# Kernel tuning notes

Measured on AMD Instinct MI355X. Metric: run time of the kernel, lower is better.

## Reference

```python
import jax, jax.numpy as jnp
import numpy as np

B, N, C = 4, 4096, 1024
NUM_HEADS = 16
HEAD_DIM = C // NUM_HEADS


def setup_inputs() -> dict:
    key = jax.random.key(0)
    k1, k2, k3, k4 = jax.random.split(key, 4)
    s_in = 1.0 / np.sqrt(C)
    return {
        "x": jax.random.normal(k1, (B, N, C), dtype=jnp.float32),
        "H": 64,
        "W": 64,
        "Wqkv": jax.random.normal(k2, (3 * C, C), dtype=jnp.float32) * s_in,
        "Wproj": jax.random.normal(k3, (C, C), dtype=jnp.float32) * s_in,
        "bproj": jnp.zeros((C,), dtype=jnp.float32),
        "alpha": jnp.ones((NUM_HEADS,), dtype=jnp.float32),
    }


def reference(x, H, W, Wqkv, Wproj, bproj, alpha):
    Bb, Nn, Cc = x.shape
    h, d = NUM_HEADS, HEAD_DIM
    # qkv: [B, N, 3C] -> [3, B, h, N, d]
    qkv = jnp.einsum('bnc,oc->bno', x, Wqkv)
    qkv = qkv.reshape(Bb, Nn, 3, h, d).transpose(2, 0, 3, 1, 4)
    q, k, v = qkv[0], qkv[1], qkv[2]  # each [B, h, N, d]
    # channel attention: contract over tokens N -> [B, h, d, d]
    attn = jnp.einsum('bhnd,bhne->bhde', k, q) / alpha[None, :, None, None]
    attn = jax.nn.softmax(attn, axis=-1)
    # (dropout is identity in eval/reference mode)
    # head_out: [B, h, d, N] -> transpose -> [B, N, h, d] -> concat heads
    out = jnp.einsum('bhde,bhne->bhdn', attn, v)
    out = out.transpose(0, 3, 1, 2).reshape(Bb, Nn, Cc)
    return jnp.einsum('bnc,oc->bno', out, Wproj) + bproj
```

## Files before the change

### kernel.cpp

```cpp
#include <hip/hip_runtime.h>
#include <hip/hip_bf16.h>
#include <cstdint>
#include <cstddef>

typedef unsigned short u16;
typedef __bf16 bf16x8 __attribute__((ext_vector_type(8)));
typedef float f32x4 __attribute__((ext_vector_type(4)));
typedef unsigned short u16x4 __attribute__((ext_vector_type(4)));
typedef unsigned short u16x8 __attribute__((ext_vector_type(8)));

#define AS1(p) ((__attribute__((address_space(1))) void*)(p))
#define AS3(p) ((__attribute__((address_space(3))) void*)(p))

__device__ __forceinline__ float bf2f(u16 u) {
  unsigned v = ((unsigned)u) << 16; float f; __builtin_memcpy(&f, &v, 4); return f;
}
__device__ __forceinline__ u16 f2bf(float f) {
  unsigned u; __builtin_memcpy(&u, &f, 4);
  u += 0x7FFFu + ((u >> 16) & 1u);
  return (u16)(u >> 16);
}

__global__ __launch_bounds__(256) void convert_kernel(const float* __restrict__ src,
                                                      u16* __restrict__ dst, int n4) {
  int i = blockIdx.x * blockDim.x + threadIdx.x;
  int stride = gridDim.x * blockDim.x;
  for (; i < n4; i += stride) {
    float4 v = ((const float4*)src)[i];
    u16x4 o;
    o.x = f2bf(v.x); o.y = f2bf(v.y); o.z = f2bf(v.z); o.w = f2bf(v.w);
    ((u16x4*)dst)[i] = o;
  }
}

__global__ __launch_bounds__(256) void convert_split_kernel(const float* __restrict__ src,
                                                            u16* __restrict__ hi,
                                                            u16* __restrict__ lo, int n4) {
  int i = blockIdx.x * blockDim.x + threadIdx.x;
  int stride = gridDim.x * blockDim.x;
  for (; i < n4; i += stride) {
    float4 v = ((const float4*)src)[i];
    u16x4 oh, ol;
    oh.x = f2bf(v.x); ol.x = f2bf(v.x - bf2f(oh.x));
    oh.y = f2bf(v.y); ol.y = f2bf(v.y - bf2f(oh.y));
    oh.z = f2bf(v.z); ol.z = f2bf(v.z - bf2f(oh.z));
    oh.w = f2bf(v.w); ol.w = f2bf(v.w - bf2f(oh.w));
    ((u16x4*)hi)[i] = oh;
    ((u16x4*)lo)[i] = ol;
  }
}

__global__ __launch_bounds__(256) void transpose_split_kernel(const float* __restrict__ x,
                                                              u16* __restrict__ Xb,
                                                              u16* __restrict__ XThi,
                                                              u16* __restrict__ XTlo) {
  __shared__ u16 lhi[64 * 72];
  __shared__ u16 llo[64 * 72];
  const int t  = threadIdx.x;
  const int nT = blockIdx.x, cT = blockIdx.y, b = blockIdx.z;
  const size_t xbase = ((size_t)b * 4096 + nT * 64) * 1024 + cT * 64;
  const int c4 = (t & 15) * 4;
  const int r0 = t >> 4;
  const int rot_w = (t & 3) << 4;
#pragma unroll
  for (int j = 0; j < 4; ++j) {
    int r = r0 + j * 16;
    float4 v = *(const float4*)(x + xbase + (size_t)r * 1024 + c4);
    u16x4 hi;
    hi.x = f2bf(v.x); hi.y = f2bf(v.y); hi.z = f2bf(v.z); hi.w = f2bf(v.w);
    *(u16x4*)(Xb + xbase + (size_t)r * 1024 + c4) = hi;
    u16 lo[4];
    lo[0] = f2bf(v.x - bf2f(hi.x)); lo[1] = f2bf(v.y - bf2f(hi.y));
    lo[2] = f2bf(v.z - bf2f(hi.z)); lo[3] = f2bf(v.w - bf2f(hi.w));
    u16 hia[4] = { hi.x, hi.y, hi.z, hi.w };
    const int rs = r ^ rot_w;
#pragma unroll
    for (int i = 0; i < 4; ++i) {
      lhi[(c4 + i) * 72 + rs] = hia[i];
      llo[(c4 + i) * 72 + rs] = lo[i];
    }
  }
  __syncthreads();
  const int c  = t >> 2;
  const int n0 = (t & 3) * 16;
  const int rot_r = ((t >> 4) & 3) << 4;
  const int nA = n0 ^ rot_r;
  const size_t tbase = ((size_t)b * 1024 + cT * 64 + c) * 4096 + nT * 64 + n0;
  *(u16x8*)(XThi + tbase)     = *(const u16x8*)(lhi + c * 72 + nA);
  *(u16x8*)(XThi + tbase + 8) = *(const u16x8*)(lhi + c * 72 + nA + 8);
  *(u16x8*)(XTlo + tbase)     = *(const u16x8*)(llo + c * 72 + nA);
  *(u16x8*)(XTlo + tbase + 8) = *(const u16x8*)(llo + c * 72 + nA + 8);
}

template<bool OUT_BF16, bool HAS_BIAS>
__global__ __launch_bounds__(512, 2) void gemm_pipe(const u16* __restrict__ A,
                                                    const u16* __restrict__ B,
                                                    void* __restrict__ Cv,
                                                    const float* __restrict__ bias,
                                                    int M, int N, int K,
                                                    size_t sA, size_t sB, size_t sC) {
  __shared__ __align__(16) u16 lds[4][2][8192];
  const int tid  = threadIdx.x;
  const int lane = tid & 63;
  const int wave = tid >> 6;
  const int wm = wave >> 2, wn = wave & 3;
  const int rowTile = blockIdx.x * 256;
  const int colTile = blockIdx.y * 256;
  A += (size_t)blockIdx.z * sA;
  B += (size_t)blockIdx.z * sB;

  size_t srcA[2], srcB[2];
  int ldsOff[2];
#pragma unroll
  for (int j = 0; j < 2; ++j) {
    const int L = j * 512 + tid;
    const int sr = L >> 3;
    const int slot = (L & 7) ^ (sr & 7);
    const int r  = (sr << 1) | (slot >> 2);
    const int kq = slot & 3;
    srcA[j] = (size_t)(rowTile + r) * K + kq * 8;
    srcB[j] = (size_t)(colTile + r) * K + kq * 8;
    ldsOff[j] = (j * 512 + (tid & 448)) * 16;
  }

  const int m15 = lane & 15, kq4 = lane >> 4;
  const int r0a = wm * 128 + m15, sa0 = r0a >> 1;
  const int idxA0 = sa0 * 64 + (((((r0a & 1) << 2) | kq4)) ^ (sa0 & 7)) * 8;
  const int r0b = wn * 64 + m15, sb0 = r0b >> 1;
  const int idxB0 = sb0 * 64 + (((((r0b & 1) << 2) | kq4)) ^ (sb0 & 7)) * 8;

  const int NT = K >> 5;

  auto stageA = [&](int tt) {
    char* d = (char*)&lds[tt & 3][0][0];
    const int kt = tt << 5;
#pragma unroll
    for (int j = 0; j < 2; ++j)
      __builtin_amdgcn_global_load_lds(AS1(A + srcA[j] + kt), AS3(d + ldsOff[j]), 16, 0, 0);
  };
  auto stageB = [&](int tt) {
    char* d = (char*)&lds[tt & 3][1][0];
    const int kt = tt << 5;
#pragma unroll
    for (int j = 0; j < 2; ++j)
      __builtin_amdgcn_global_load_lds(AS1(B + srcB[j] + kt), AS3(d + ldsOff[j]), 16, 0, 0);
  };

  stageA(0); stageB(0);
  if (NT > 1) { stageA(1); stageB(1); }
  if (NT > 2) { stageA(2); stageB(2); }
  if (NT > 2) asm volatile("s_waitcnt vmcnt(8)" ::: "memory");
  else        asm volatile("s_waitcnt vmcnt(0)" ::: "memory");
  __builtin_amdgcn_sched_barrier(0);
  __builtin_amdgcn_s_barrier();
  __builtin_amdgcn_sched_barrier(0);

  f32x4 acc[8][4] = {};
  for (int t = 0; t < NT; ++t) {
    const u16* bufA = &lds[t & 3][0][0];
    const u16* bufB = &lds[t & 3][1][0];
    bf16x8 a[8], bfr[4];
#pragma unroll
    for (int ni = 0; ni < 4; ++ni) bfr[ni] = *(const bf16x8*)(bufB + idxB0 + ni * 512);
#pragma unroll
    for (int mi = 0; mi < 4; ++mi) a[mi] = *(const bf16x8*)(bufA + idxA0 + mi * 512);
    if (t + 3 < NT) stageA(t + 3);
    __builtin_amdgcn_sched_barrier(0);
    __builtin_amdgcn_s_barrier();
    __builtin_amdgcn_sched_barrier(0);
    __builtin_amdgcn_s_setprio(1);
#pragma unroll
    for (int mi = 0; mi < 4; ++mi)
#pragma unroll
      for (int ni = 0; ni < 4; ++ni)
        acc[mi][ni] = __builtin_amdgcn_mfma_f32_16x16x32_bf16(a[mi], bfr[ni], acc[mi][ni], 0, 0, 0);
    __builtin_amdgcn_s_setprio(0);
    __builtin_amdgcn_sched_barrier(0);
    __builtin_amdgcn_s_barrier();
    __builtin_amdgcn_sched_barrier(0);
#pragma unroll
    for (int mi = 4; mi < 8; ++mi) a[mi] = *(const bf16x8*)(bufA + idxA0 + mi * 512);
    if (t + 3 < NT) stageB(t + 3);
    __builtin_amdgcn_sched_barrier(0);
    __builtin_amdgcn_s_barrier();
    __builtin_amdgcn_sched_barrier(0);
    __builtin_amdgcn_s_setprio(1);
#pragma unroll
    for (int mi = 4; mi < 8; ++mi)
#pragma unroll
      for (int ni = 0; ni < 4; ++ni)
        acc[mi][ni] = __builtin_amdgcn_mfma_f32_16x16x32_bf16(a[mi], bfr[ni], acc[mi][ni], 0, 0, 0);
    __builtin_amdgcn_s_setprio(0);
    if (t < NT - 1) {
      if (t + 3 < NT)      asm volatile("s_waitcnt vmcnt(8)" ::: "memory");
      else if (t + 2 < NT) asm volatile("s_waitcnt vmcnt(4)" ::: "memory");
      else                 asm volatile("s_waitcnt vmcnt(0)" ::: "memory");
    }
    __builtin_amdgcn_sched_barrier(0);
    __builtin_amdgcn_s_barrier();
    __builtin_amdgcn_sched_barrier(0);
  }

  const int crow0 = rowTile + wm * 128 + (lane >> 4) * 4;
  const int ccol0 = colTile + wn * 64 + m15;
  if constexpr (OUT_BF16) {
    u16* C = (u16*)Cv + (size_t)blockIdx.z * sC;
#pragma unroll
    for (int mi = 0; mi < 8; ++mi)
#pragma unroll
      for (int ni = 0; ni < 4; ++ni) {
        const int col = ccol0 + ni * 16;
        const float bv = HAS_BIAS ? bias[col] : 0.f;
#pragma unroll
        for (int r = 0; r < 4; ++r)
          C[(size_t)(crow0 + mi * 16 + r) * N + col] = f2bf(acc[mi][ni][r] + bv);
      }
  } else {
    float* C = (float*)Cv + (size_t)blockIdx.z * sC;
#pragma unroll
    for (int mi = 0; mi < 8; ++mi)
#pragma unroll
      for (int ni = 0; ni < 4; ++ni) {
        const int col = ccol0 + ni * 16;
        const float bv = HAS_BIAS ? bias[col] : 0.f;
#pragma unroll
        for (int r = 0; r < 4; ++r)
          C[(size_t)(crow0 + mi * 16 + r) * N + col] = acc[mi][ni][r] + bv;
      }
  }
}

template<int L>
__device__ __forceinline__ void pipe4k_core(const u16* __restrict__ pAh,
                                            const u16* __restrict__ pAl,
                                            const u16* __restrict__ pBh,
                                            const u16* __restrict__ pBl,
                                            u16* lds, int ldsByteOff,
                                            int idxA0, int idxB0, int bOff,
                                            int NT, int half,
                                            f32x4 acc[4][4]) {
  auto stage = [&](int tt) {
    u16* d = lds + (tt & 3) * 16384;
    const int kt = tt << 5;
    __builtin_amdgcn_global_load_lds(AS1(pAh + kt), AS3((char*)d + ldsByteOff), 16, 0, 0);
    __builtin_amdgcn_global_load_lds(AS1(pAl + kt), AS3((char*)(d + 4096) + ldsByteOff), 16, 0, 0);
    if constexpr (L == 4) {
      __builtin_amdgcn_global_load_lds(AS1(pBh + kt), AS3((char*)(d + 8192) + ldsByteOff), 16, 0, 0);
      __builtin_amdgcn_global_load_lds(AS1(pBl + kt), AS3((char*)(d + 12288) + ldsByteOff), 16, 0, 0);
    }
  };

  stage(0); stage(1); stage(2); stage(3);
  if constexpr (L == 4) asm volatile("s_waitcnt vmcnt(8)" ::: "memory");
  else                  asm volatile("s_waitcnt vmcnt(4)" ::: "memory");
  __builtin_amdgcn_sched_barrier(0);
  __builtin_amdgcn_s_barrier();
  __builtin_amdgcn_sched_barrier(0);

  const int npairs = NT >> 1;
  for (int i = 0; i < npairs; ++i) {
    const u16* base = lds + ((2 * i + half) & 3) * 16384;
    bf16x8 ah[4], al[4], bh[4], bl[4];
#pragma unroll
    for (int ni = 0; ni < 4; ++ni) {
      bh[ni] = *(const bf16x8*)(base + bOff + idxB0 + ni * 512);
      bl[ni] = *(const bf16x8*)(base + bOff + 4096 + idxB0 + ni * 512);
    }
    ah[0] = *(const bf16x8*)(base + idxA0);
    ah[1] = *(const bf16x8*)(base + idxA0 + 512);
    al[0] = *(const bf16x8*)(base + 4096 + idxA0);
    al[1] = *(const bf16x8*)(base + 4096 + idxA0 + 512);
    __builtin_amdgcn_sched_barrier(0);
    __builtin_amdgcn_s_barrier();
    __builtin_amdgcn_sched_barrier(0);
    __builtin_amdgcn_s_setprio(1);
#pragma unroll
    for (int mi = 0; mi < 2; ++mi)
#pragma unroll
      for (int ni = 0; ni < 4; ++ni) {
        acc[mi][ni] = __builtin_amdgcn_mfma_f32_16x16x32_bf16(ah[mi], bh[ni], acc[mi][ni], 0, 0, 0);
        acc[mi][ni] = __builtin_amdgcn_mfma_f32_16x16x32_bf16(ah[mi], bl[ni], acc[mi][ni], 0, 0, 0);
        acc[mi][ni] = __builtin_amdgcn_mfma_f32_16x16x32_bf16(al[mi], bh[ni], acc[mi][ni], 0, 0, 0);
      }
    __builtin_amdgcn_s_setprio(0);
    __builtin_amdgcn_sched_barrier(0);
    __builtin_amdgcn_s_barrier();
    __builtin_amdgcn_sched_barrier(0);
    ah[2] = *(const bf16x8*)(base + idxA0 + 1024);
    ah[3] = *(const bf16x8*)(base + idxA0 + 1536);
    al[2] = *(const bf16x8*)(base + 4096 + idxA0 + 1024);
    al[3] = *(const bf16x8*)(base + 4096 + idxA0 + 1536);
    __builtin_amdgcn_sched_barrier(0);
    __builtin_amdgcn_s_barrier();
    __builtin_amdgcn_sched_barrier(0);
    if (i + 2 < npairs) { stage(2 * i + 4); stage(2 * i + 5); }
    __builtin_amdgcn_sched_barrier(0);
    __builtin_amdgcn_s_setprio(1);
#pragma unroll
    for (int mi = 2; mi < 4; ++mi)
#pragma unroll
      for (int ni = 0; ni < 4; ++ni) {
        acc[mi][ni] = __builtin_amdgcn_mfma_f32_16x16x32_bf16(ah[mi], bh[ni], acc[mi][ni], 0, 0, 0);
        acc[mi][ni] = __builtin_amdgcn_mfma_f32_16x16x32_bf16(ah[mi], bl[ni], acc[mi][ni], 0, 0, 0);
        acc[mi][ni] = __builtin_amdgcn_mfma_f32_16x16x32_bf16(al[mi], bh[ni], acc[mi][ni], 0, 0, 0);
      }
    __builtin_amdgcn_s_setprio(0);
    if (i < npairs - 1) {
      if (i + 2 < npairs) {
        if constexpr (L == 4) asm volatile("s_waitcnt vmcnt(8)" ::: "memory");
        else                  asm volatile("s_waitcnt vmcnt(4)" ::: "memory");
      } else {
        asm volatile("s_waitcnt vmcnt(0)" ::: "memory");
      }
    }
    __builtin_amdgcn_sched_barrier(0);
    __builtin_amdgcn_s_barrier();
    __builtin_amdgcn_sched_barrier(0);
  }
}

__global__ __launch_bounds__(512, 2) void gram_pipe(const u16* __restrict__ XThi,
                                                    const u16* __restrict__ XTlo,
                                                    float* __restrict__ Gpart) {
  __shared__ __align__(16) u16 ldsmem[4 * 4 * 4096];
  const int tid = threadIdx.x, lane = tid & 63, wave = tid >> 6;
  const int q = wave & 3, half = wave >> 2;
  const int qm = q >> 1, qn = q & 1;
  const int bid = blockIdx.x;
  int b, rT, cT, slice, k0, NT; bool same = false;
  if (bid < 64) {
    b = bid & 3; const int j2 = bid >> 2;
    rT = cT = j2 >> 1; slice = j2 & 1; k0 = slice * 2048; NT = 64; same = true;
  } else {
    const int e = bid - 64; b = e & 3;
    const int idx = e >> 2; const int tile = idx >> 2, kq = idx & 3;
    int t = tile, rt = 0;
    while (t >= 7 - rt) { t -= 7 - rt; ++rt; }
    const int ct = rt + 1 + t;
    rT = rt; cT = ct;
    if (kq >= 2) { rT = ct; cT = rt; }
    slice = kq & 1; k0 = kq * 1024; NT = 32;
  }
  const int rowTile = rT * 128, colTile = cT * 128;
  const u16* Ah = XThi + ((size_t)b << 22);
  const u16* Al = XTlo + ((size_t)b << 22);

  const int sr = tid >> 3;
  const int slot = (tid & 7) ^ (sr & 7);
  const int r = (sr << 1) | (slot >> 2);
  const int kq8 = (slot & 3) * 8;
  const u16* pAh = Ah + (size_t)(rowTile + r) * 4096 + k0 + kq8;
  const u16* pAl = Al + (size_t)(rowTile + r) * 4096 + k0 + kq8;
  const u16* pBh = Ah + (size_t)(colTile + r) * 4096 + k0 + kq8;
  const u16* pBl = Al + (size_t)(colTile + r) * 4096 + k0 + kq8;
  const int ldsByteOff = (tid & 448) * 16;

  const int m15 = lane & 15, kq4 = lane >> 4;
  const int r0a = qm * 64 + m15, sa0 = r0a >> 1;
  const int idxA0 = sa0 * 64 + (((((r0a & 1) << 2) | kq4)) ^ (sa0 & 7)) * 8;
  const int r0b = qn * 64 + m15, sb0 = r0b >> 1;
  const int idxB0 = sb0 * 64 + (((((r0b & 1) << 2) | kq4)) ^ (sb0 & 7)) * 8;

  f32x4 acc[4][4] = {};
  if (same) pipe4k_core<2>(pAh, pAl, pAh, pAl, ldsmem, ldsByteOff, idxA0, idxB0, 0, NT, half, acc);
  else      pipe4k_core<4>(pAh, pAl, pBh, pBl, ldsmem, ldsByteOff, idxA0, idxB0, 8192, NT, half, acc);

  float* red = (float*)ldsmem;
  const int rr = (lane >> 4) * 4;
  if (half) {
#pragma unroll
    for (int mi = 0; mi < 4; ++mi)
#pragma unroll
      for (int ni = 0; ni < 4; ++ni)
        *(f32x4*)(red + q * 4352 + (ni * 16 + m15) * 68 + mi * 16 + rr) = acc[mi][ni];
  }
  __syncthreads();
  if (!half) {
    float* out = Gpart + ((size_t)(slice * 4 + b) << 20);
    const int crow0 = rowTile + qm * 64 + rr;
    const int ccol0 = colTile + qn * 64 + m15;
#pragma unroll
    for (int mi = 0; mi < 4; ++mi)
#pragma unroll
      for (int ni = 0; ni < 4; ++ni) {
        f32x4 v = *(const f32x4*)(red + q * 4352 + (ni * 16 + m15) * 68 + mi * 16 + rr);
        v += acc[mi][ni];
#pragma unroll
        for (int r4 = 0; r4 < 4; ++r4)
          out[(size_t)(crow0 + mi * 16 + r4) * 1024 + ccol0 + ni * 16] = v[r4];
      }
  }
}

__global__ __launch_bounds__(256) void gram_reduce_split(const float* __restrict__ Gp,
                                                         u16* __restrict__ Ghi,
                                                         u16* __restrict__ Glo) {
  const int rt = blockIdx.x, ct = blockIdx.y, b = blockIdx.z;
  const bool diag128 = (rt >> 1) == (ct >> 1);
  const float* s0 = Gp + ((size_t)b << 20);
  const float* s1 = Gp + ((size_t)(4 + b) << 20);
  __shared__ float lT[64 * 68];
  const int t = threadIdx.x;
  const int r = t >> 2;
  const int c16 = (t & 3) * 16;

  if (!diag128) {
    const size_t bb = (size_t)(ct * 64 + r) * 1024 + rt * 64 + c16;
#pragma unroll
    for (int q = 0; q < 4; ++q) {
      float4 v0 = *(const float4*)(s0 + bb + q * 4);
      float4 v1 = *(const float4*)(s1 + bb + q * 4);
      float4 s = { v0.x + v1.x, v0.y + v1.y, v0.z + v1.z, v0.w + v1.w };
      *(float4*)(lT + r * 68 + c16 + q * 4) = s;
    }
    __syncthreads();
  }

  const size_t ab = (size_t)(rt * 64 + r) * 1024 + ct * 64 + c16;
  const size_t ob = ((size_t)b << 20) + ab;
#pragma unroll
  for (int q = 0; q < 4; ++q) {
    float4 v0 = *(const float4*)(s0 + ab + q * 4);
    float4 v1 = *(const float4*)(s1 + ab + q * 4);
    float g[4] = { v0.x + v1.x, v0.y + v1.y, v0.z + v1.z, v0.w + v1.w };
    if (!diag128) {
#pragma unroll
      for (int i = 0; i < 4; ++i) g[i] += lT[(c16 + q * 4 + i) * 68 + r];
    }
    u16x4 oh, ol;
    oh.x = f2bf(g[0]); ol.x = f2bf(g[0] - bf2f(oh.x));
    oh.y = f2bf(g[1]); ol.y = f2bf(g[1] - bf2f(oh.y));
    oh.z = f2bf(g[2]); ol.z = f2bf(g[2] - bf2f(oh.z));
    oh.w = f2bf(g[3]); ol.w = f2bf(g[3] - bf2f(oh.w));
    *(u16x4*)(Ghi + ob + q * 4) = oh;
    *(u16x4*)(Glo + ob + q * 4) = ol;
  }
}

__global__ __launch_bounds__(512, 2) void tprime_pipe(const u16* __restrict__ Wqh,
                                                      const u16* __restrict__ Wql,
                                                      const u16* __restrict__ Ghi,
                                                      const u16* __restrict__ Glo,
                                                      u16* __restrict__ Tph,
                                                      u16* __restrict__ Tpl) {
  __shared__ __align__(16) u16 ldsmem[4 * 4 * 4096];
  const int tid = threadIdx.x, lane = tid & 63, wave = tid >> 6;
  const int q = wave & 3, half = wave >> 2;
  const int qm = q >> 1, qn = q & 1;
  const int bid = blockIdx.x;
  const int b = bid & 3, tile = bid >> 2;
  const int rowTile = (tile >> 3) * 128, colTile = (tile & 7) * 128;
  const size_t zoff = (size_t)b << 20;

  const int sr = tid >> 3;
  const int slot = (tid & 7) ^ (sr & 7);
  const int r = (sr << 1) | (slot >> 2);
  const int kq8 = (slot & 3) * 8;
  const u16* pAh = Wqh + (size_t)(rowTile + r) * 1024 + kq8;
  const u16* pAl = Wql + (size_t)(rowTile + r) * 1024 + kq8;
  const u16* pBh = Ghi + zoff + (size_t)(colTile + r) * 1024 + kq8;
  const u16* pBl = Glo + zoff + (size_t)(colTile + r) * 1024 + kq8;
  const int ldsByteOff = (tid & 448) * 16;

  const int m15 = lane & 15, kq4 = lane >> 4;
  const int r0a = qm * 64 + m15, sa0 = r0a >> 1;
  const int idxA0 = sa0 * 64 + (((((r0a & 1) << 2) | kq4)) ^ (sa0 & 7)) * 8;
  const int r0b = qn * 64 + m15, sb0 = r0b >> 1;
  const int idxB0 = sb0 * 64 + (((((r0b & 1) << 2) | kq4)) ^ (sb0 & 7)) * 8;

  f32x4 acc[4][4] = {};
  pipe4k_core<4>(pAh, pAl, pBh, pBl, ldsmem, ldsByteOff, idxA0, idxB0, 8192, 32, half, acc);

  float* red = (float*)ldsmem;
  const int rr = (lane >> 4) * 4;
  if (half) {
#pragma unroll
    for (int mi = 0; mi < 4; ++mi)
#pragma unroll
      for (int ni = 0; ni < 4; ++ni)
        *(f32x4*)(red + q * 4352 + (ni * 16 + m15) * 68 + mi * 16 + rr) = acc[mi][ni];
  }
  __syncthreads();
  if (!half) {
    const int crow0 = rowTile + qm * 64 + rr;
    const int ccol0 = colTile + qn * 64 + m15;
#pragma unroll
    for (int mi = 0; mi < 4; ++mi)
#pragma unroll
      for (int ni = 0; ni < 4; ++ni) {
        f32x4 v = *(const f32x4*)(red + q * 4352 + (ni * 16 + m15) * 68 + mi * 16 + rr);
        v += acc[mi][ni];
#pragma unroll
        for (int r4 = 0; r4 < 4; ++r4) {
          float x = v[r4];
          u16 hi = f2bf(x);
          u16 lo = f2bf(x - bf2f(hi));
          size_t off = zoff + (size_t)(crow0 + mi * 16 + r4) * 1024 + ccol0 + ni * 16;
          Tph[off] = hi;
          Tpl[off] = lo;
        }
      }
  }
}

__global__ __launch_bounds__(256) void s_softmax_kernel(const u16* __restrict__ Wqh,
                                                        const u16* __restrict__ Wql,
                                                        const u16* __restrict__ Tph,
                                                        const u16* __restrict__ Tpl,
                                                        const float* __restrict__ alpha,
                                                        u16* __restrict__ attnT) {
  const int h = blockIdx.x, b = blockIdx.y;
  const int tid = threadIdx.x, lane = tid & 63, wave = tid >> 6;
  __shared__ __align__(16) u16 lAh[64 * 32];
  __shared__ __align__(16) u16 lAl[64 * 32];
  __shared__ __align__(16) u16 lBh[64 * 32];
  __shared__ __align__(16) u16 lBl[64 * 32];

  const size_t aBase = (size_t)(1024 + h * 64) * 1024;
  const size_t bBase = ((size_t)b << 20) + (size_t)(h * 64) * 1024;

  f32x4 acc[4] = {};
  const int m  = lane & 15;
  const int ko = (lane >> 4) * 8;
  const int srow = tid >> 2;
  const int skc  = (tid & 3) * 8;
  const int ldsOff = (tid & 192) * 16;

  for (int kt = 0; kt < 1024; kt += 32) {
    __builtin_amdgcn_global_load_lds(AS1(Wqh + aBase + (size_t)srow * 1024 + kt + skc),
                                     AS3((char*)lAh + ldsOff), 16, 0, 0);
    __builtin_amdgcn_global_load_lds(AS1(Wql + aBase + (size_t)srow * 1024 + kt + skc),
                                     AS3((char*)lAl + ldsOff), 16, 0, 0);
    __builtin_amdgcn_global_load_lds(AS1(Tph + bBase + (size_t)srow * 1024 + kt + skc),
                                     AS3((char*)lBh + ldsOff), 16, 0, 0);
    __builtin_amdgcn_global_load_lds(AS1(Tpl + bBase + (size_t)srow * 1024 + kt + skc),
                                     AS3((char*)lBl + ldsOff), 16, 0, 0);
    __syncthreads();
    bf16x8 ah = *(const bf16x8*)(lAh + (wave * 16 + m) * 32 + ko);
    bf16x8 al = *(const bf16x8*)(lAl + (wave * 16 + m) * 32 + ko);
#pragma unroll
    for (int cb = 0; cb < 4; ++cb) {
      bf16x8 bh = *(const bf16x8*)(lBh + (cb * 16 + m) * 32 + ko);
      bf16x8 bl = *(const bf16x8*)(lBl + (cb * 16 + m) * 32 + ko);
      acc[cb] = __builtin_amdgcn_mfma_f32_16x16x32_bf16(ah, bh, acc[cb], 0, 0, 0);
      acc[cb] = __builtin_amdgcn_mfma_f32_16x16x32_bf16(ah, bl, acc[cb], 0, 0, 0);
      acc[cb] = __builtin_amdgcn_mfma_f32_16x16x32_bf16(al, bh, acc[cb], 0, 0, 0);
    }
    __syncthreads();
  }

  const float invA = 1.f / alpha[h];
  const int g = lane >> 4;
  const size_t obase = (size_t)(b * 16 + h) * 4096;
#pragma unroll
  for (int r = 0; r < 4; ++r) {
    int d = wave * 16 + g * 4 + r;
    float s[4];
#pragma unroll
    for (int cb = 0; cb < 4; ++cb) s[cb] = acc[cb][r] * invA;
    float mx = fmaxf(fmaxf(s[0], s[1]), fmaxf(s[2], s[3]));
#pragma unroll
    for (int o = 1; o < 16; o <<= 1) mx = fmaxf(mx, __shfl_xor(mx, o, 64));
    float e[4]; float sum = 0.f;
#pragma unroll
    for (int cb = 0; cb < 4; ++cb) { e[cb] = __expf(s[cb] - mx); sum += e[cb]; }
#pragma unroll
    for (int o = 1; o < 16; o <<= 1) sum += __shfl_xor(sum, o, 64);
    float inv = 1.f / sum;
#pragma unroll
    for (int cb = 0; cb < 4; ++cb) {
      int e_idx = cb * 16 + (lane & 15);
      attnT[obase + (size_t)e_idx * 64 + d] = f2bf(e[cb] * inv);
    }
  }
}

__global__ __launch_bounds__(256) void m_build_kernel(const u16* __restrict__ Wpb,
                                                      const u16* __restrict__ attnT,
                                                      u16* __restrict__ Mb) {
  const int oT = blockIdx.x, h = blockIdx.y, b = blockIdx.z;
  const int tid = threadIdx.x, lane = tid & 63, wave = tid >> 6;
  __shared__ __align__(16) u16 lA[128 * 64];
  __shared__ __align__(16) u16 lB[64 * 64];
  const int bh = b * 16 + h;
#pragma unroll
  for (int i = 0; i < 4; ++i) {
    int idx = i * 256 + tid;
    int row = idx >> 3;
    int kc  = (idx & 7) * 8;
    int ldsOff = (i * 256 + (tid & 192)) * 16;
    __builtin_amdgcn_global_load_lds(AS1(Wpb + (size_t)(oT * 128 + row) * 1024 + h * 64 + kc),
                                     AS3((char*)lA + ldsOff), 16, 0, 0);
  }
#pragma unroll
  for (int i = 0; i < 2; ++i) {
    int idx = i * 256 + tid;
    int ldsOff = (i * 256 + (tid & 192)) * 16;
    __builtin_amdgcn_global_load_lds(AS1(attnT + (size_t)bh * 4096 + idx * 8),
                                     AS3((char*)lB + ldsOff), 16, 0, 0);
  }
  __syncthreads();
  const int m  = lane & 15;
  const int ko = (lane >> 4) * 8;
  const int wr = wave * 32;
  f32x4 acc[2][4] = {};
#pragma unroll
  for (int ks = 0; ks < 2; ++ks) {
#pragma unroll
    for (int rb = 0; rb < 2; ++rb) {
      bf16x8 a = *(const bf16x8*)(lA + (wr + rb * 16 + m) * 64 + ks * 32 + ko);
#pragma unroll
      for (int cb = 0; cb < 4; ++cb) {
        bf16x8 bb = *(const bf16x8*)(lB + (cb * 16 + m) * 64 + ks * 32 + ko);
        acc[rb][cb] = __builtin_amdgcn_mfma_f32_16x16x32_bf16(a, bb, acc[rb][cb], 0, 0, 0);
      }
    }
  }
  u16* out = Mb + ((size_t)b << 20);
#pragma unroll
  for (int rb = 0; rb < 2; ++rb)
#pragma unroll
    for (int cb = 0; cb < 4; ++cb) {
      int col = h * 64 + cb * 16 + (lane & 15);
#pragma unroll
      for (int r = 0; r < 4; ++r) {
        int row = oT * 128 + wr + rb * 16 + (lane >> 4) * 4 + r;
        out[(size_t)row * 1024 + col] = f2bf(acc[rb][cb][r]);
      }
    }
}

extern "C" void kernel_launch(void* const* d_in, const int* in_sizes, int n_in,
                              void* d_out, int out_size, void* d_ws, size_t ws_size,
                              hipStream_t stream) {
  const float* x     = (const float*)d_in[0];
  const float* Wqkv  = (const float*)d_in[3];
  const float* Wproj = (const float*)d_in[4];
  const float* bproj = (const float*)d_in[5];
  const float* alpha = (const float*)d_in[6];

  char* ws = (char*)d_ws;
  u16*   Xb     = (u16*)ws;
  float* Gpart  = (float*)ws;
  u16*   Mb     = (u16*)ws;
  u16*   XThi   = (u16*)(ws + 33554432);
  u16*   attnTb = (u16*)(ws + 33554432);
  u16*   XTlo  = (u16*)(ws + 67108864);
  u16*   Ghi   = (u16*)(ws + 67108864);
  u16*   Glo   = (u16*)(ws + 75497472);
  u16*   Tph   = (u16*)(ws + 83886080);
  u16*   Tpl   = (u16*)(ws + 92274688);
  u16*   Wqh   = (u16*)(ws + 100663296);
  u16*   Wql   = (u16*)(ws + 106954752);
  u16*   Vb    = (u16*)(ws + 113246208);
  u16*   Wpb   = (u16*)(ws + 146800640);

  transpose_split_kernel<<<dim3(64, 16, 4), 256, 0, stream>>>(x, Xb, XThi, XTlo);
  convert_split_kernel<<<256, 256, 0, stream>>>(Wqkv, Wqh, Wql, 3145728 / 4);
  convert_kernel<<<128, 256, 0, stream>>>(Wproj, Wpb, 1048576 / 4);
  gemm_pipe<true, false><<<dim3(64, 4, 1), 512, 0, stream>>>(
      Xb, Wqh + (size_t)2048 * 1024, Vb, nullptr, 16384, 1024, 1024,
      (size_t)0, (size_t)0, (size_t)0);
  gram_pipe<<<dim3(512), 512, 0, stream>>>(XThi, XTlo, Gpart);
  gram_reduce_split<<<dim3(16, 16, 4), 256, 0, stream>>>(Gpart, Ghi, Glo);
  tprime_pipe<<<dim3(256), 512, 0, stream>>>(Wqh, Wql, Ghi, Glo, Tph, Tpl);
  s_softmax_kernel<<<dim3(16, 4), 256, 0, stream>>>(Wqh, Wql, Tph, Tpl, alpha, attnTb);
  m_build_kernel<<<dim3(8, 16, 4), 256, 0, stream>>>(Wpb, attnTb, Mb);
  gemm_pipe<false, true><<<dim3(16, 4, 4), 512, 0, stream>>>(
      Vb, Mb, (float*)d_out, bproj, 4096, 1024, 1024,
      (size_t)1 << 22, (size_t)1 << 20, (size_t)1 << 22);
}
```

Before: 381.9 us.

## Split tprime tile across 8 waves without K-split and parallelize s_softmax K loop

The tprime kernel stops splitting K across two half-block wave groups with an LDS reduction. Instead each of the 8 waves owns a 64x32 output sub-tile, fed by a new 4-stage pipelined core that interleaves A/B staging with two MFMA phases. This removes the reduction pass and its extra sync, at the cost of more LDS fragment reads per MFMA. The s_softmax kernel moves to 512 threads that split K into even/odd chunks across two halves with swizzled LDS, then reduces through LDS before the softmax, aiming to shorten its serial K loop on its tiny 64-block grid.

```diff
diff --git a/kernel.cpp b/kernel.cpp
--- a/kernel.cpp
+++ b/kernel.cpp
@@ -227,6 +227,101 @@
         for (int r = 0; r < 4; ++r)
           C[(size_t)(crow0 + mi * 16 + r) * N + col] = acc[mi][ni][r] + bv;
       }
+  }
+}
+
+template<int L>
+__device__ __forceinline__ void pipe4_core(const u16* __restrict__ pAh,
+                                           const u16* __restrict__ pAl,
+                                           const u16* __restrict__ pBh,
+                                           const u16* __restrict__ pBl,
+                                           u16* lds, int ldsByteOff,
+                                           int idxA0, int idxB0, int bOff, int NT,
+                                           f32x4 acc[4][2]) {
+  auto stage2A = [&](int tt) {
+    u16* d = lds + (tt & 3) * 16384;
+    const int kt = tt << 5;
+    __builtin_amdgcn_global_load_lds(AS1(pAh + kt), AS3((char*)d + ldsByteOff), 16, 0, 0);
+    __builtin_amdgcn_global_load_lds(AS1(pAl + kt), AS3((char*)(d + 4096) + ldsByteOff), 16, 0, 0);
+  };
+  auto stage2B = [&](int tt) {
+    if constexpr (L == 4) {
+      u16* d = lds + (tt & 3) * 16384 + 8192;
+      const int kt = tt << 5;
+      __builtin_amdgcn_global_load_lds(AS1(pBh + kt), AS3((char*)d + ldsByteOff), 16, 0, 0);
+      __builtin_amdgcn_global_load_lds(AS1(pBl + kt), AS3((char*)(d + 4096) + ldsByteOff), 16, 0, 0);
+    }
+  };
+
+  stage2A(0); stage2B(0);
+  stage2A(1); stage2B(1);
+  stage2A(2); stage2B(2);
+  if constexpr (L == 4) asm volatile("s_waitcnt vmcnt(8)" ::: "memory");
+  else                  asm volatile("s_waitcnt vmcnt(4)" ::: "memory");
+  __builtin_amdgcn_sched_barrier(0);
+  __builtin_amdgcn_s_barrier();
+  __builtin_amdgcn_sched_barrier(0);
+
+  for (int t = 0; t < NT; ++t) {
+    const u16* base = lds + (t & 3) * 16384;
+    bf16x8 ah[4], al[4], bh[2], bl[2];
+    bh[0] = *(const bf16x8*)(base + bOff + idxB0);
+    bh[1] = *(const bf16x8*)(base + bOff + idxB0 + 512);
+    bl[0] = *(const bf16x8*)(base + bOff + 4096 + idxB0);
+    bl[1] = *(const bf16x8*)(base + bOff + 4096 + idxB0 + 512);
+    ah[0] = *(const bf16x8*)(base + idxA0);
+    ah[1] = *(const bf16x8*)(base + idxA0 + 512);
+    al[0] = *(const bf16x8*)(base + 4096 + idxA0);
+    al[1] = *(const bf16x8*)(base + 4096 + idxA0 + 512);
+    if (t + 3 < NT) stage2A(t + 3);
+    __builtin_amdgcn_sched_barrier(0);
+    __builtin_amdgcn_s_barrier();
+    __builtin_amdgcn_sched_barrier(0);
+    __builtin_amdgcn_s_setprio(1);
+#pragma unroll
+    for (int mi = 0; mi < 2; ++mi)
+#pragma unroll
+      for (int ni = 0; ni < 2; ++ni) {
+        acc[mi][ni] = __builtin_amdgcn_mfma_f32_16x16x32_bf16(ah[mi], bh[ni], acc[mi][ni], 0, 0, 0);
+        acc[mi][ni] = __builtin_amdgcn_mfma_f32_16x16x32_bf16(ah[mi], bl[ni], acc[mi][ni], 0, 0, 0);
+        acc[mi][ni] = __builtin_amdgcn_mfma_f32_16x16x32_bf16(al[mi], bh[ni], acc[mi][ni], 0, 0, 0);
+      }
+    __builtin_amdgcn_s_setprio(0);
+    __builtin_amdgcn_sched_barrier(0);
+    __builtin_amdgcn_s_barrier();
+    __builtin_amdgcn_sched_barrier(0);
+    ah[2] = *(const bf16x8*)(base + idxA0 + 1024);
+    ah[3] = *(const bf16x8*)(base + idxA0 + 1536);
+    al[2] = *(const bf16x8*)(base + 4096 + idxA0 + 1024);
+    al[3] = *(const bf16x8*)(base + 4096 + idxA0 + 1536);
+    if (t + 3 < NT) stage2B(t + 3);
+    __builtin_amdgcn_sched_barrier(0);
+    __builtin_amdgcn_s_barrier();
+    __builtin_amdgcn_sched_barrier(0);
+    __builtin_amdgcn_s_setprio(1);
+#pragma unroll
+    for (int mi = 2; mi < 4; ++mi)
+#pragma unroll
+      for (int ni = 0; ni < 2; ++ni) {
+        acc[mi][ni] = __builtin_amdgcn_mfma_f32_16x16x32_bf16(ah[mi], bh[ni], acc[mi][ni], 0, 0, 0);
+        acc[mi][ni] = __builtin_amdgcn_mfma_f32_16x16x32_bf16(ah[mi], bl[ni], acc[mi][ni], 0, 0, 0);
+        acc[mi][ni] = __builtin_amdgcn_mfma_f32_16x16x32_bf16(al[mi], bh[ni], acc[mi][ni], 0, 0, 0);
+      }
+    __builtin_amdgcn_s_setprio(0);
+    if (t < NT - 1) {
+      if constexpr (L == 4) {
+        if (t + 3 < NT)      asm volatile("s_waitcnt vmcnt(8)" ::: "memory");
+        else if (t + 2 < NT) asm volatile("s_waitcnt vmcnt(4)" ::: "memory");
+        else                 asm volatile("s_waitcnt vmcnt(0)" ::: "memory");
+      } else {
+        if (t + 3 < NT)      asm volatile("s_waitcnt vmcnt(4)" ::: "memory");
+        else if (t + 2 < NT) asm volatile("s_waitcnt vmcnt(2)" ::: "memory");
+        else                 asm volatile("s_waitcnt vmcnt(0)" ::: "memory");
+      }
+    }
+    __builtin_amdgcn_sched_barrier(0);
+    __builtin_amdgcn_s_barrier();
+    __builtin_amdgcn_sched_barrier(0);
   }
 }
 
@@ -443,10 +538,9 @@
                                                       const u16* __restrict__ Glo,
                                                       u16* __restrict__ Tph,
                                                       u16* __restrict__ Tpl) {
-  __shared__ __align__(16) u16 ldsmem[4 * 4 * 4096];
+  __shared__ __align__(16) u16 lds[4 * 4 * 4096];
   const int tid = threadIdx.x, lane = tid & 63, wave = tid >> 6;
-  const int q = wave & 3, half = wave >> 2;
-  const int qm = q >> 1, qn = q & 1;
+  const int wm = wave >> 2, wn = wave & 3;
   const int bid = blockIdx.x;
   const int b = bid & 3, tile = bid >> 2;
   const int rowTile = (tile >> 3) * 128, colTile = (tile & 7) * 128;
@@ -463,47 +557,32 @@
   const int ldsByteOff = (tid & 448) * 16;
 
   const int m15 = lane & 15, kq4 = lane >> 4;
-  const int r0a = qm * 64 + m15, sa0 = r0a >> 1;
+  const int r0a = wm * 64 + m15, sa0 = r0a >> 1;
   const int idxA0 = sa0 * 64 + (((((r0a & 1) << 2) | kq4)) ^ (sa0 & 7)) * 8;
-  const int r0b = qn * 64 + m15, sb0 = r0b >> 1;
+  const int r0b = wn * 32 + m15, sb0 = r0b >> 1;
   const int idxB0 = sb0 * 64 + (((((r0b & 1) << 2) | kq4)) ^ (sb0 & 7)) * 8;
 
-  f32x4 acc[4][4] = {};
-  pipe4k_core<4>(pAh, pAl, pBh, pBl, ldsmem, ldsByteOff, idxA0, idxB0, 8192, 32, half, acc);
-
-  float* red = (float*)ldsmem;
-  const int rr = (lane >> 4) * 4;
-  if (half) {
-#pragma unroll
-    for (int mi = 0; mi < 4; ++mi)
-#pragma unroll
-      for (int ni = 0; ni < 4; ++ni)
-        *(f32x4*)(red + q * 4352 + (ni * 16 + m15) * 68 + mi * 16 + rr) = acc[mi][ni];
-  }
-  __syncthreads();
-  if (!half) {
-    const int crow0 = rowTile + qm * 64 + rr;
-    const int ccol0 = colTile + qn * 64 + m15;
-#pragma unroll
-    for (int mi = 0; mi < 4; ++mi)
-#pragma unroll
-      for (int ni = 0; ni < 4; ++ni) {
-        f32x4 v = *(const f32x4*)(red + q * 4352 + (ni * 16 + m15) * 68 + mi * 16 + rr);
-        v += acc[mi][ni];
-#pragma unroll
-        for (int r4 = 0; r4 < 4; ++r4) {
-          float x = v[r4];
-          u16 hi = f2bf(x);
-          u16 lo = f2bf(x - bf2f(hi));
-          size_t off = zoff + (size_t)(crow0 + mi * 16 + r4) * 1024 + ccol0 + ni * 16;
-          Tph[off] = hi;
-          Tpl[off] = lo;
-        }
-      }
-  }
-}
-
-__global__ __launch_bounds__(256) void s_softmax_kernel(const u16* __restrict__ Wqh,
+  f32x4 acc[4][2] = {};
+  pipe4_core<4>(pAh, pAl, pBh, pBl, lds, ldsByteOff, idxA0, idxB0, 8192, 32, acc);
+
+  const int crow0 = rowTile + wm * 64 + (lane >> 4) * 4;
+  const int ccol0 = colTile + wn * 32 + m15;
+#pragma unroll
+  for (int mi = 0; mi < 4; ++mi)
+#pragma unroll
+    for (int ni = 0; ni < 2; ++ni)
+#pragma unroll
+      for (int r4 = 0; r4 < 4; ++r4) {
+        float v = acc[mi][ni][r4];
+        u16 hi = f2bf(v);
+        u16 lo = f2bf(v - bf2f(hi));
+        size_t off = zoff + (size_t)(crow0 + mi * 16 + r4) * 1024 + ccol0 + ni * 16;
+        Tph[off] = hi;
+        Tpl[off] = lo;
+      }
+}
+
+__global__ __launch_bounds__(512) void s_softmax_kernel(const u16* __restrict__ Wqh,
                                                         const u16* __restrict__ Wql,
                                                         const u16* __restrict__ Tph,
                                                         const u16* __restrict__ Tpl,
@@ -511,37 +590,47 @@
                                                         u16* __restrict__ attnT) {
   const int h = blockIdx.x, b = blockIdx.y;
   const int tid = threadIdx.x, lane = tid & 63, wave = tid >> 6;
-  __shared__ __align__(16) u16 lAh[64 * 32];
-  __shared__ __align__(16) u16 lAl[64 * 32];
-  __shared__ __align__(16) u16 lBh[64 * 32];
-  __shared__ __align__(16) u16 lBl[64 * 32];
+  const int half = wave >> 2, w4 = wave & 3;
+  __shared__ __align__(16) u16 sm[2][4][64 * 32];
 
   const size_t aBase = (size_t)(1024 + h * 64) * 1024;
   const size_t bBase = ((size_t)b << 20) + (size_t)(h * 64) * 1024;
 
+  const int tid2 = tid & 255;
+  const int sr = tid2 >> 3;
+  const int slot = (tid2 & 7) ^ (sr & 7);
+  const int r = (sr << 1) | (slot >> 2);
+  const int kq8 = (slot & 3) * 8;
+  const u16* pAh = Wqh + aBase + (size_t)r * 1024 + kq8;
+  const u16* pAl = Wql + aBase + (size_t)r * 1024 + kq8;
+  const u16* pBh = Tph + bBase + (size_t)r * 1024 + kq8;
+  const u16* pBl = Tpl + bBase + (size_t)r * 1024 + kq8;
+  const int off = (tid2 & 192) * 16;
+
+  const int m = lane & 15, kq4 = lane >> 4;
+  const int rA = w4 * 16 + m, sA0 = rA >> 1;
+  const int idxA = sA0 * 64 + (((((rA & 1) << 2) | kq4)) ^ (sA0 & 7)) * 8;
+  int idxB[4];
+#pragma unroll
+  for (int cb = 0; cb < 4; ++cb) {
+    const int rB = cb * 16 + m, sB0 = rB >> 1;
+    idxB[cb] = sB0 * 64 + (((((rB & 1) << 2) | kq4)) ^ (sB0 & 7)) * 8;
+  }
+
   f32x4 acc[4] = {};
-  const int m  = lane & 15;
-  const int ko = (lane >> 4) * 8;
-  const int srow = tid >> 2;
-  const int skc  = (tid & 3) * 8;
-  const int ldsOff = (tid & 192) * 16;
-
-  for (int kt = 0; kt < 1024; kt += 32) {
-    __builtin_amdgcn_global_load_lds(AS1(Wqh + aBase + (size_t)srow * 1024 + kt + skc),
-                                     AS3((char*)lAh + ldsOff), 16, 0, 0);
-    __builtin_amdgcn_global_load_lds(AS1(Wql + aBase + (size_t)srow * 1024 + kt + skc),
-                                     AS3((char*)lAl + ldsOff), 16, 0, 0);
-    __builtin_amdgcn_global_load_lds(AS1(Tph + bBase + (size_t)srow * 1024 + kt + skc),
-                                     AS3((char*)lBh + ldsOff), 16, 0, 0);
-    __builtin_amdgcn_global_load_lds(AS1(Tpl + bBase + (size_t)srow * 1024 + kt + skc),
-                                     AS3((char*)lBl + ldsOff), 16, 0, 0);
+  for (int i = 0; i < 16; ++i) {
+    const int kt = (2 * i + half) * 32;
+    __builtin_amdgcn_global_load_lds(AS1(pAh + kt), AS3((char*)&sm[half][0][0] + off), 16, 0, 0);
+    __builtin_amdgcn_global_load_lds(AS1(pAl + kt), AS3((char*)&sm[half][1][0] + off), 16, 0, 0);
+    __builtin_amdgcn_global_load_lds(AS1(pBh + kt), AS3((char*)&sm[half][2][0] + off), 16, 0, 0);
+    __builtin_amdgcn_global_load_lds(AS1(pBl + kt), AS3((char*)&sm[half][3][0] + off), 16, 0, 0);
     __syncthreads();
-    bf16x8 ah = *(const bf16x8*)(lAh + (wave * 16 + m) * 32 + ko);
-    bf16x8 al = *(const bf16x8*)(lAl + (wave * 16 + m) * 32 + ko);
+    bf16x8 ah = *(const bf16x8*)(&sm[half][0][0] + idxA);
+    bf16x8 al = *(const bf16x8*)(&sm[half][1][0] + idxA);
 #pragma unroll
     for (int cb = 0; cb < 4; ++cb) {
-      bf16x8 bh = *(const bf16x8*)(lBh + (cb * 16 + m) * 32 + ko);
-      bf16x8 bl = *(const bf16x8*)(lBl + (cb * 16 + m) * 32 + ko);
+      bf16x8 bh = *(const bf16x8*)(&sm[half][2][0] + idxB[cb]);
+      bf16x8 bl = *(const bf16x8*)(&sm[half][3][0] + idxB[cb]);
       acc[cb] = __builtin_amdgcn_mfma_f32_16x16x32_bf16(ah, bh, acc[cb], 0, 0, 0);
       acc[cb] = __builtin_amdgcn_mfma_f32_16x16x32_bf16(ah, bl, acc[cb], 0, 0, 0);
       acc[cb] = __builtin_amdgcn_mfma_f32_16x16x32_bf16(al, bh, acc[cb], 0, 0, 0);
@@ -549,28 +638,42 @@
     __syncthreads();
   }
 
-  const float invA = 1.f / alpha[h];
-  const int g = lane >> 4;
-  const size_t obase = (size_t)(b * 16 + h) * 4096;
-#pragma unroll
-  for (int r = 0; r < 4; ++r) {
-    int d = wave * 16 + g * 4 + r;
-    float s[4];
-#pragma unroll
-    for (int cb = 0; cb < 4; ++cb) s[cb] = acc[cb][r] * invA;
-    float mx = fmaxf(fmaxf(s[0], s[1]), fmaxf(s[2], s[3]));
-#pragma unroll
-    for (int o = 1; o < 16; o <<= 1) mx = fmaxf(mx, __shfl_xor(mx, o, 64));
-    float e[4]; float sum = 0.f;
-#pragma unroll
-    for (int cb = 0; cb < 4; ++cb) { e[cb] = __expf(s[cb] - mx); sum += e[cb]; }
-#pragma unroll
-    for (int o = 1; o < 16; o <<= 1) sum += __shfl_xor(sum, o, 64);
-    float inv = 1.f / sum;
-#pragma unroll
-    for (int cb = 0; cb < 4; ++cb) {
-      int e_idx = cb * 16 + (lane & 15);
-      attnT[obase + (size_t)e_idx * 64 + d] = f2bf(e[cb] * inv);
+  float* red = (float*)&sm[0][0][0];
+  const int rbase = (w4 * 64 + lane) * 20;
+  if (half) {
+#pragma unroll
+    for (int cb = 0; cb < 4; ++cb)
+      *(f32x4*)(red + rbase + cb * 4) = acc[cb];
+  }
+  __syncthreads();
+  if (!half) {
+#pragma unroll
+    for (int cb = 0; cb < 4; ++cb)
+      acc[cb] += *(const f32x4*)(red + rbase + cb * 4);
+
+    const float invA = 1.f / alpha[h];
+    const int g = lane >> 4;
+    const size_t obase = (size_t)(b * 16 + h) * 4096;
+#pragma unroll
+    for (int rr = 0; rr < 4; ++rr) {
+      int d = w4 * 16 + g * 4 + rr;
+      float s[4];
+#pragma unroll
+      for (int cb = 0; cb < 4; ++cb) s[cb] = acc[cb][rr] * invA;
+      float mx = fmaxf(fmaxf(s[0], s[1]), fmaxf(s[2], s[3]));
+#pragma unroll
+      for (int o = 1; o < 16; o <<= 1) mx = fmaxf(mx, __shfl_xor(mx, o, 64));
+      float e[4]; float sum = 0.f;
+#pragma unroll
+      for (int cb = 0; cb < 4; ++cb) { e[cb] = __expf(s[cb] - mx); sum += e[cb]; }
+#pragma unroll
+      for (int o = 1; o < 16; o <<= 1) sum += __shfl_xor(sum, o, 64);
+      float inv = 1.f / sum;
+#pragma unroll
+      for (int cb = 0; cb < 4; ++cb) {
+        int e_idx = cb * 16 + (lane & 15);
+        attnT[obase + (size_t)e_idx * 64 + d] = f2bf(e[cb] * inv);
+      }
     }
   }
 }
@@ -664,7 +767,7 @@
   gram_pipe<<<dim3(512), 512, 0, stream>>>(XThi, XTlo, Gpart);
   gram_reduce_split<<<dim3(16, 16, 4), 256, 0, stream>>>(Gpart, Ghi, Glo);
   tprime_pipe<<<dim3(256), 512, 0, stream>>>(Wqh, Wql, Ghi, Glo, Tph, Tpl);
-  s_softmax_kernel<<<dim3(16, 4), 256, 0, stream>>>(Wqh, Wql, Tph, Tpl, alpha, attnTb);
+  s_softmax_kernel<<<dim3(16, 4), 512, 0, stream>>>(Wqh, Wql, Tph, Tpl, alpha, attnTb);
   m_build_kernel<<<dim3(8, 16, 4), 256, 0, stream>>>(Wpb, attnTb, Mb);
   gemm_pipe<false, true><<<dim3(16, 4, 4), 512, 0, stream>>>(
       Vb, Mb, (float*)d_out, bproj, 4096, 1024, 1024,
```

Result: faster. 369.0 us (-3.4%).
